# Optimization experiments

Measured on AMD Instinct MI355X. Metric: run time of the kernel, lower is better.

The kernel has to match this reference:

```python
import jax, jax.numpy as jnp
import numpy as np

B, S, DIM = 2, 1024, 1024
N_EXPERTS, K = 8, 2
VOCAB = 16384
HIDDEN = DIM * 8 // 3          # 2730
UP_OUT = HIDDEN * 2            # 5460 (swiglu doubling)


def setup_inputs() -> dict:
    key = jax.random.key(0)
    ks = jax.random.split(key, 5)
    x = jax.random.normal(ks[0], (B, S, DIM), dtype=jnp.float32)
    w_router = jax.random.normal(ks[1], (N_EXPERTS, DIM), dtype=jnp.float32) * 0.02
    w_up = jax.random.normal(ks[2], (N_EXPERTS, UP_OUT, DIM), dtype=jnp.float32) * 0.02
    w_down = jax.random.normal(ks[3], (N_EXPERTS, DIM, HIDDEN), dtype=jnp.float32) * 0.02
    w_proj = jax.random.normal(ks[4], (N_EXPERTS, VOCAB, DIM), dtype=jnp.float32) * 0.02
    return {"x": x, "w_router": w_router, "w_up": w_up, "w_down": w_down, "w_proj": w_proj}


def _grouped_linear(x_sorted, weight, group_sizes):
    # weight: [n_experts, out, in] (torch Linear layout) -> ragged_dot wants [g, in, out]
    return jax.lax.ragged_dot(x_sorted, jnp.swapaxes(weight, 1, 2), group_sizes)


def reference(x, w_router, w_up, w_down, w_proj):
    b, s, d = x.shape
    # Router (eval path): plain top-k of linear scores
    scores = jnp.einsum("bsd,nd->bsn", x, w_router)
    c, ids = jax.lax.top_k(scores, K)                   # [B,S,K]
    # Dispatch: replicate tokens k times, sort by expert id (stable, matching torch.sort)
    xe = jnp.broadcast_to(x[..., None, :], (b, s, K, d)).reshape(-1, d)   # [T, d]
    ids_flat = ids.reshape(-1)
    order = jnp.argsort(ids_flat)                        # stable sort indices
    x_sorted = xe[order]
    group_sizes = jnp.bincount(ids_flat, length=N_EXPERTS).astype(jnp.int32)
    # Expert swiglu MLP with residual (grouped GEMMs)
    skip = x_sorted
    h = _grouped_linear(x_sorted, w_up, group_sizes)     # [T, 2*HIDDEN]
    h_lin, h_gate = jnp.split(h, 2, axis=-1)
    h = h_lin * jax.nn.silu(h_gate)
    h = _grouped_linear(h, w_down, group_sizes) + skip   # [T, d]
    logits = _grouped_linear(h, w_proj, group_sizes)     # [T, VOCAB]
    # Postprocess: scatter back to original token order
    out = jnp.zeros_like(logits).at[order].set(logits)
    out = out.reshape(b, s, K, VOCAB)
    # Weighted top-k combine
    w = jax.nn.softmax(c, axis=-1)                       # [B,S,K]
    return jnp.sum(out * w[..., None], axis=-2)          # [B,S,VOCAB]
```

## Files before the change

### kernel.cpp

```cpp
#include <hip/hip_runtime.h>
#include <hip/hip_bf16.h>

typedef __bf16 bf16_t;
typedef __bf16 bf16x2 __attribute__((ext_vector_type(2)));
typedef __bf16 bf16x4 __attribute__((ext_vector_type(4)));
typedef __bf16 bf16x8 __attribute__((ext_vector_type(8)));
typedef float f32x4 __attribute__((ext_vector_type(4)));

#define DIM     1024
#define NEXP    8
#define VOCAB   16384
#define HIDDEN  2730
#define UPOUT   5460
#define NTOK    2048
#define NSLOT   4096
#define HRAW_LD 5472
#define H1_LD   2752
#define BM      256
#define MAXTILES 24

#define WS_COUNTS      0
#define WS_NTILES      64
#define WS_TILE_E      128
#define WS_TILE_M0     256
#define WS_TILE_MEND   384
#define WS_SLOT_IDS    1024
#define WS_SLOT_W      20480
#define WS_SLOT_OF_POS 40960
#define WS_POS_OF_SLOT 61440
#define WS_XSORTED     131072
#define WS_H2          8519680
#define WS_H1          16908288
#define WS_HRAW        39452672
#define WS_LOGITS      16908288ull
#define WS_NEED_BIG    (WS_LOGITS + (size_t)NSLOT * VOCAB * 2)

__device__ __forceinline__ void gload_lds16(const void* g, void* l) {
    __builtin_amdgcn_global_load_lds((const __attribute__((address_space(1))) void*)g,
                                     (__attribute__((address_space(3))) void*)l, 16, 0, 0);
}
__device__ __forceinline__ int swzm(int r) { return (r ^ (r >> 2)) & 3; }

__global__ __launch_bounds__(256) void router_kernel(const float* __restrict__ x,
        const float* __restrict__ wr, int* __restrict__ slot_ids,
        float* __restrict__ slot_w, int* __restrict__ counts) {
    const int lane = threadIdx.x & 63;
    const int wave = threadIdx.x >> 6;
    const int token = blockIdx.x * 4 + wave;
    const float* xrow = x + (size_t)token * DIM;
    float acc[NEXP];
#pragma unroll
    for (int e = 0; e < NEXP; ++e) acc[e] = 0.f;
#pragma unroll
    for (int i = 0; i < DIM / 64; ++i) {
        const int k = i * 64 + lane;
        const float xv = xrow[k];
#pragma unroll
        for (int e = 0; e < NEXP; ++e) acc[e] += xv * wr[e * DIM + k];
    }
#pragma unroll
    for (int off = 32; off > 0; off >>= 1) {
#pragma unroll
        for (int e = 0; e < NEXP; ++e) acc[e] += __shfl_xor(acc[e], off);
    }
    if (lane == 0) {
        float c0 = -1e30f; int b0 = 0;
#pragma unroll
        for (int e = 0; e < NEXP; ++e) if (acc[e] > c0) { c0 = acc[e]; b0 = e; }
        float c1 = -1e30f; int b1 = 0;
#pragma unroll
        for (int e = 0; e < NEXP; ++e) if (e != b0 && acc[e] > c1) { c1 = acc[e]; b1 = e; }
        slot_ids[token * 2 + 0] = b0;
        slot_ids[token * 2 + 1] = b1;
        const float w0 = 1.f / (1.f + expf(c1 - c0));
        slot_w[token * 2 + 0] = w0;
        slot_w[token * 2 + 1] = 1.f - w0;
        atomicAdd(&counts[b0], 1);
        atomicAdd(&counts[b1], 1);
    }
}

__global__ __launch_bounds__(512) void sched_kernel(const int* __restrict__ counts,
        int* __restrict__ ntiles, int* __restrict__ tile_e, int* __restrict__ tile_m0,
        int* __restrict__ tile_mend, const int* __restrict__ slot_ids,
        int* __restrict__ slot_of_pos, int* __restrict__ pos_of_slot) {
    __shared__ int offs[NEXP];
    if (threadIdx.x == 0) {
        int o = 0, nt = 0;
        for (int e = 0; e < NEXP; ++e) {
            offs[e] = o;
            const int c = counts[e];
            for (int m = 0; m < c; m += BM) {
                tile_e[nt] = e; tile_m0[nt] = o + m; tile_mend[nt] = o + c; ++nt;
            }
            o += c;
        }
        *ntiles = nt;
    }
    __syncthreads();
    const int e = threadIdx.x >> 6;
    const int lane = threadIdx.x & 63;
    int base = offs[e];
    for (int ch = 0; ch < NSLOT / 64; ++ch) {
        const int i = ch * 64 + lane;
        const int id = slot_ids[i];
        const unsigned long long m = __ballot(id == e);
        if (id == e) {
            const int rank = __popcll(m & ((1ull << lane) - 1ull));
            slot_of_pos[base + rank] = i;
            pos_of_slot[i] = base + rank;
        }
        base += __popcll(m);
    }
}

__global__ __launch_bounds__(256) void gather_kernel(const float* __restrict__ x,
        const int* __restrict__ slot_of_pos, bf16_t* __restrict__ xs) {
    const int row = blockIdx.x;
    const int t = threadIdx.x;
    const int tok = slot_of_pos[row] >> 1;
    const float4 v = *(const float4*)(x + (size_t)tok * DIM + t * 4);
    bf16x4 o;
    o.x = (bf16_t)v.x; o.y = (bf16_t)v.y; o.z = (bf16_t)v.z; o.w = (bf16_t)v.w;
    *(bf16x4*)(xs + (size_t)row * DIM + t * 4) = o;
}

__global__ __launch_bounds__(256) void swiglu_kernel(const bf16_t* __restrict__ hraw,
        bf16_t* __restrict__ h1) {
    const int row = blockIdx.x;
    const int col = blockIdx.y * 256 + threadIdx.x;
    if (col >= H1_LD) return;
    float o = 0.f;
    if (col < HIDDEN) {
        const float a = (float)hraw[(size_t)row * HRAW_LD + col];
        const float g = (float)hraw[(size_t)row * HRAW_LD + col + HIDDEN];
        o = a * (g / (1.f + expf(-g)));
    }
    h1[(size_t)row * H1_LD + col] = (bf16_t)o;
}

__global__ __launch_bounds__(256) void combine_kernel(const bf16_t* __restrict__ logits,
        const int* __restrict__ pos_of_slot, const float* __restrict__ slot_w,
        float* __restrict__ out) {
    const int t = blockIdx.x;
    const int v0 = (blockIdx.y * 256 + threadIdx.x) * 8;
    const int p0 = pos_of_slot[2 * t], p1 = pos_of_slot[2 * t + 1];
    const float w0 = slot_w[2 * t], w1 = slot_w[2 * t + 1];
    const bf16x8 a = *(const bf16x8*)(logits + (size_t)p0 * VOCAB + v0);
    const bf16x8 b = *(const bf16x8*)(logits + (size_t)p1 * VOCAB + v0);
    float o[8];
#pragma unroll
    for (int i = 0; i < 8; ++i) o[i] = w0 * (float)a[i] + w1 * (float)b[i];
    *(float4*)(out + (size_t)t * VOCAB + v0)     = make_float4(o[0], o[1], o[2], o[3]);
    *(float4*)(out + (size_t)t * VOCAB + v0 + 4) = make_float4(o[4], o[5], o[6], o[7]);
}

template <int EPI, bool BW16, int BN, bool SWZ>
__global__ __launch_bounds__(1024, 4) void gemm_kernel(
        const bf16_t* __restrict__ A, int lda,
        const float* __restrict__ B, int N, int K, int KT, long bLast,
        bf16_t* __restrict__ C, int ldc,
        const bf16_t* __restrict__ skip,
        const int* __restrict__ slot_of_pos,
        const float* __restrict__ slot_w,
        float* __restrict__ outp,
        const int* __restrict__ tile_e,
        const int* __restrict__ tile_m0,
        const int* __restrict__ tile_mend,
        const int* __restrict__ ntiles) {
    if (blockIdx.y >= (unsigned)*ntiles) return;
    int bx = blockIdx.x;
    if constexpr (SWZ) bx = (bx & 7) * (gridDim.x >> 3) + (bx >> 3);
    const int e = tile_e[blockIdx.y];
    const int m0 = tile_m0[blockIdx.y];
    const int mend = tile_mend[blockIdx.y];
    const int n0 = bx * BN;

    constexpr int NI = BN / 64;
    constexpr int NB = BW16 ? BN / 128 : 1;
    constexpr int VM = NB + 1;

    __shared__ bf16_t sA[2][BM][32];
    __shared__ bf16_t sB[2][BN][32];

    const int tid = threadIdx.x;
    const int lane = tid & 63;
    const int wave = tid >> 6;
    const int wr = wave >> 2;
    const int wc = wave & 3;
    const int fr = lane & 15;
    const int fq = lane >> 4;

    f32x4 acc[4][NI] = {};

    auto stageA = [&](int buf, int kt) {
        const int k0 = min(kt, KT - 1) * 32;
        const int rb = wave * 16;
        const int r = rb + (lane >> 2);
        const int gr = min(m0 + r, NSLOT - 1);
        const int c16 = (lane & 3) ^ swzm(r);
        gload_lds16(A + (size_t)gr * lda + k0 + c16 * 8, &sA[buf][rb][0]);
    };
    auto loadB = [&](int kt, f32x4* va, float2& vc) {
        const int k0 = min(kt, KT - 1) * 32;
        if constexpr (BW16) {
#pragma unroll
            for (int nb = 0; nb < NB; ++nb) {
                const int gr = min(n0 + nb * 128 + wave * 8 + (lane >> 3), N - 1);
                va[nb] = *(const f32x4*)(B + (size_t)e * N * K + (size_t)gr * K
                                         + k0 + (lane & 7) * 4);
            }
        } else {
            long fl = (long)e * N * K + (long)(n0 + wave * 4 + (lane >> 4)) * K
                      + k0 + (lane & 15) * 2;
            if (fl > bLast) fl = bLast;
            vc = *(const float2*)(B + fl);
        }
    };
    auto writeB = [&](int buf, const f32x4* va, const float2& vc) {
        if constexpr (BW16) {
#pragma unroll
            for (int nb = 0; nb < NB; ++nb) {
                const int r = nb * 128 + wave * 8 + (lane >> 3);
                bf16x4 t;
                t.x = (bf16_t)va[nb].x; t.y = (bf16_t)va[nb].y;
                t.z = (bf16_t)va[nb].z; t.w = (bf16_t)va[nb].w;
                char* p = (char*)&sB[buf][r][0]
                        + ((((lane & 7) >> 1) ^ swzm(r)) * 16) + (lane & 1) * 8;
                *(bf16x4*)p = t;
            }
        } else {
            const int r = wave * 4 + (lane >> 4);
            bf16x2 t; t.x = (bf16_t)vc.x; t.y = (bf16_t)vc.y;
            const int q = lane & 15;
            char* p = (char*)&sB[buf][r][0] + (((q >> 2) ^ swzm(r)) * 16) + (q & 3) * 4;
            *(bf16x2*)p = t;
        }
    };
    auto compute = [&](int buf) {
        bf16x8 bb[NI];
#pragma unroll
        for (int ni = 0; ni < NI; ++ni) {
            const int r = wc * (BN / 4) + ni * 16 + fr;
            bb[ni] = *(const bf16x8*)&sB[buf][r][(fq ^ swzm(r)) * 8];
        }
        __builtin_amdgcn_s_setprio(1);
#pragma unroll
        for (int mi = 0; mi < 4; ++mi) {
            const int r = wr * 64 + mi * 16 + fr;
            const bf16x8 af = *(const bf16x8*)&sA[buf][r][(fq ^ swzm(r)) * 8];
#pragma unroll
            for (int ni = 0; ni < NI; ++ni)
                acc[mi][ni] = __builtin_amdgcn_mfma_f32_16x16x32_bf16(
                        af, bb[ni], acc[mi][ni], 0, 0, 0);
        }
        __builtin_amdgcn_s_setprio(0);
    };

    f32x4 Pa[NB], Qa[NB]; float2 Pc, Qc;
    loadB(0, Pa, Pc);
    stageA(0, 0);
    loadB(1, Qa, Qc);
    asm volatile("s_waitcnt vmcnt(%0)" :: "n"(VM) : "memory");
    writeB(0, Pa, Pc);
    asm volatile("s_waitcnt lgkmcnt(0)" ::: "memory");
    stageA(1, 1);

    for (int kt = 0; kt < KT; kt += 2) {
        loadB(kt + 2, Pa, Pc);
        asm volatile("s_waitcnt vmcnt(%0)" :: "n"(VM) : "memory");
        __builtin_amdgcn_s_barrier();
        asm volatile("" ::: "memory");
        writeB(1, Qa, Qc);
        compute(0);
        asm volatile("s_waitcnt lgkmcnt(0)" ::: "memory");
        __builtin_amdgcn_s_barrier();
        asm volatile("" ::: "memory");
        stageA(0, kt + 2);
        loadB(kt + 3, Qa, Qc);
        asm volatile("s_waitcnt vmcnt(%0)" :: "n"(VM) : "memory");
        __builtin_amdgcn_s_barrier();
        asm volatile("" ::: "memory");
        writeB(0, Pa, Pc);
        compute(1);
        asm volatile("s_waitcnt lgkmcnt(0)" ::: "memory");
        __builtin_amdgcn_s_barrier();
        asm volatile("" ::: "memory");
        stageA(1, kt + 3);
    }

#pragma unroll
    for (int mi = 0; mi < 4; ++mi) {
#pragma unroll
        for (int reg = 0; reg < 4; ++reg) {
            const int r = m0 + wr * 64 + mi * 16 + fq * 4 + reg;
            if (r >= mend) continue;
            int tok = 0; float wgt = 0.f;
            if constexpr (EPI == 2) {
                const int slot = slot_of_pos[r];
                tok = slot >> 1;
                wgt = slot_w[slot];
            }
#pragma unroll
            for (int ni = 0; ni < NI; ++ni) {
                const int c = n0 + wc * (BN / 4) + ni * 16 + fr;
                if (c >= N) continue;
                float v = acc[mi][ni][reg];
                if constexpr (EPI == 0) {
                    C[(size_t)r * ldc + c] = (bf16_t)v;
                } else if constexpr (EPI == 1) {
                    v += (float)skip[(size_t)r * DIM + c];
                    C[(size_t)r * ldc + c] = (bf16_t)v;
                } else {
                    unsafeAtomicAdd(&outp[(size_t)tok * VOCAB + c], v * wgt);
                }
            }
        }
    }
}

extern "C" void kernel_launch(void* const* d_in, const int* in_sizes, int n_in,
                              void* d_out, int out_size, void* d_ws, size_t ws_size,
                              hipStream_t stream) {
    const float* x        = (const float*)d_in[0];
    const float* w_router = (const float*)d_in[1];
    const float* w_up     = (const float*)d_in[2];
    const float* w_down   = (const float*)d_in[3];
    const float* w_proj   = (const float*)d_in[4];
    float* out = (float*)d_out;
    char* ws = (char*)d_ws;

    int*    counts      = (int*)(ws + WS_COUNTS);
    int*    ntiles      = (int*)(ws + WS_NTILES);
    int*    tile_e      = (int*)(ws + WS_TILE_E);
    int*    tile_m0     = (int*)(ws + WS_TILE_M0);
    int*    tile_mend   = (int*)(ws + WS_TILE_MEND);
    int*    slot_ids    = (int*)(ws + WS_SLOT_IDS);
    float*  slot_w      = (float*)(ws + WS_SLOT_W);
    int*    slot_of_pos = (int*)(ws + WS_SLOT_OF_POS);
    int*    pos_of_slot = (int*)(ws + WS_POS_OF_SLOT);
    bf16_t* x_sorted    = (bf16_t*)(ws + WS_XSORTED);
    bf16_t* h2          = (bf16_t*)(ws + WS_H2);
    bf16_t* h1          = (bf16_t*)(ws + WS_H1);
    bf16_t* h_raw       = (bf16_t*)(ws + WS_HRAW);
    bf16_t* logits      = (bf16_t*)(ws + WS_LOGITS);

    const bool bigws = ws_size >= WS_NEED_BIG;

    hipMemsetAsync(d_ws, 0, 1024, stream);

    router_kernel<<<NTOK / 4, 256, 0, stream>>>(x, w_router, slot_ids, slot_w, counts);
    sched_kernel<<<1, 512, 0, stream>>>(counts, ntiles, tile_e, tile_m0, tile_mend,
                                        slot_ids, slot_of_pos, pos_of_slot);
    gather_kernel<<<NSLOT, 256, 0, stream>>>(x, slot_of_pos, x_sorted);

    gemm_kernel<0, true, 256, false><<<dim3((UPOUT + 255) / 256, MAXTILES), 1024, 0, stream>>>(
        x_sorted, DIM, w_up, UPOUT, DIM, 32, 0,
        h_raw, HRAW_LD,
        nullptr, nullptr, nullptr, nullptr, tile_e, tile_m0, tile_mend, ntiles);

    swiglu_kernel<<<dim3(NSLOT, (H1_LD + 255) / 256), 256, 0, stream>>>(h_raw, h1);

    gemm_kernel<1, false, 64, true><<<dim3(DIM / 64, MAXTILES), 1024, 0, stream>>>(
        h1, H1_LD, w_down, DIM, HIDDEN, (HIDDEN + 31) / 32,
        (long)NEXP * DIM * HIDDEN - 2,
        h2, DIM,
        x_sorted, nullptr, nullptr, nullptr, tile_e, tile_m0, tile_mend, ntiles);

    if (bigws) {
        gemm_kernel<0, true, 256, true><<<dim3(VOCAB / 256, MAXTILES), 1024, 0, stream>>>(
            h2, DIM, w_proj, VOCAB, DIM, 32, 0,
            logits, VOCAB,
            nullptr, nullptr, nullptr, nullptr, tile_e, tile_m0, tile_mend, ntiles);
        combine_kernel<<<dim3(NTOK, VOCAB / (256 * 8)), 256, 0, stream>>>(
            logits, pos_of_slot, slot_w, out);
    } else {
        hipMemsetAsync(d_out, 0, (size_t)out_size * sizeof(float), stream);
        gemm_kernel<2, true, 256, true><<<dim3(VOCAB / 256, MAXTILES), 1024, 0, stream>>>(
            h2, DIM, w_proj, VOCAB, DIM, 32, 0,
            nullptr, 0,
            nullptr, slot_of_pos, slot_w, out, tile_e, tile_m0, tile_mend, ntiles);
    }
}
```

Baseline: 631.4 us.

## Split GEMM into 512-thread high-reuse kernel and specialized mid kernel

Adds a dedicated gemm_hi kernel for the up and vocab projections. It uses 512 threads per block, so each wave computes an 8x4 grid of MFMA tiles instead of 4x4, which raises register-level reuse of the A and B fragments. Its B loads are rewritten so each thread reads 16 contiguous floats and writes them as two 16-byte bf16x8 stores to LDS. The down projection moves to a trimmed gemm_mid kernel that preloads all A fragments before the MFMA loop. The cost is higher register pressure in gemm_hi (128 accumulator floats per thread), fewer waves resident per CU, and more LDS work per thread.

```diff
diff --git a/kernel.cpp b/kernel.cpp
--- a/kernel.cpp
+++ b/kernel.cpp
@@ -155,15 +155,158 @@
     *(float4*)(out + (size_t)t * VOCAB + v0 + 4) = make_float4(o[4], o[5], o[6], o[7]);
 }
 
-template <int EPI, bool BW16, int BN, bool SWZ>
-__global__ __launch_bounds__(1024, 4) void gemm_kernel(
+template <int EPI, bool SWZ>
+__global__ __launch_bounds__(512, 2) void gemm_hi(
+        const bf16_t* __restrict__ A,
+        const float* __restrict__ B, int N,
+        bf16_t* __restrict__ C, int ldc,
+        const int* __restrict__ slot_of_pos,
+        const float* __restrict__ slot_w,
+        float* __restrict__ outp,
+        const int* __restrict__ tile_e,
+        const int* __restrict__ tile_m0,
+        const int* __restrict__ tile_mend,
+        const int* __restrict__ ntiles) {
+    if (blockIdx.y >= (unsigned)*ntiles) return;
+    constexpr int K = 1024, KT = 32;
+    int bx = blockIdx.x;
+    if constexpr (SWZ) bx = (bx & 7) * (gridDim.x >> 3) + (bx >> 3);
+    const int e = tile_e[blockIdx.y];
+    const int m0 = tile_m0[blockIdx.y];
+    const int mend = tile_mend[blockIdx.y];
+    const int n0 = bx * 256;
+    const float* __restrict__ Bexp = B + (size_t)e * N * K;
+
+    __shared__ bf16_t sA[2][256][32];
+    __shared__ bf16_t sB[2][256][32];
+
+    const int tid = threadIdx.x;
+    const int lane = tid & 63;
+    const int wave = tid >> 6;
+    const int wr = wave >> 2;
+    const int wc = wave & 3;
+    const int fr = lane & 15;
+    const int fq = lane >> 4;
+
+    const int brow = tid >> 1;
+    const int bseg = tid & 1;
+    const float* bsrc = Bexp + (size_t)min(n0 + brow, N - 1) * K + bseg * 16;
+
+    f32x4 acc[8][4] = {};
+
+    auto stageA = [&](int buf, int kt) {
+        const int k0 = min(kt, KT - 1) * 32;
+#pragma unroll
+        for (int j = 0; j < 2; ++j) {
+            const int rb = wave * 32 + j * 16;
+            const int r = rb + (lane >> 2);
+            const int gr = min(m0 + r, NSLOT - 1);
+            const int c16 = (lane & 3) ^ swzm(r);
+            gload_lds16(A + (size_t)gr * K + k0 + c16 * 8, &sA[buf][rb][0]);
+        }
+    };
+    auto loadB = [&](int kt, f32x4* v) {
+        const int k0 = min(kt, KT - 1) * 32;
+#pragma unroll
+        for (int j = 0; j < 4; ++j) v[j] = *(const f32x4*)(bsrc + k0 + j * 4);
+    };
+    auto writeB = [&](int buf, const f32x4* v) {
+#pragma unroll
+        for (int u = 0; u < 2; ++u) {
+            bf16x8 t;
+            t[0] = (bf16_t)v[2*u][0]; t[1] = (bf16_t)v[2*u][1];
+            t[2] = (bf16_t)v[2*u][2]; t[3] = (bf16_t)v[2*u][3];
+            t[4] = (bf16_t)v[2*u+1][0]; t[5] = (bf16_t)v[2*u+1][1];
+            t[6] = (bf16_t)v[2*u+1][2]; t[7] = (bf16_t)v[2*u+1][3];
+            const int unit = (bseg * 2 + u) ^ swzm(brow);
+            *(bf16x8*)&sB[buf][brow][unit * 8] = t;
+        }
+    };
+    auto compute = [&](int buf) {
+        bf16x8 bb[4];
+#pragma unroll
+        for (int ni = 0; ni < 4; ++ni) {
+            const int r = wc * 64 + ni * 16 + fr;
+            bb[ni] = *(const bf16x8*)&sB[buf][r][(fq ^ swzm(r)) * 8];
+        }
+        __builtin_amdgcn_s_setprio(1);
+#pragma unroll
+        for (int mi = 0; mi < 8; ++mi) {
+            const int r = wr * 128 + mi * 16 + fr;
+            const bf16x8 af = *(const bf16x8*)&sA[buf][r][(fq ^ swzm(r)) * 8];
+#pragma unroll
+            for (int ni = 0; ni < 4; ++ni)
+                acc[mi][ni] = __builtin_amdgcn_mfma_f32_16x16x32_bf16(
+                        af, bb[ni], acc[mi][ni], 0, 0, 0);
+        }
+        __builtin_amdgcn_s_setprio(0);
+    };
+
+    f32x4 P[4], Q[4];
+    loadB(0, P);
+    stageA(0, 0);
+    loadB(1, Q);
+    asm volatile("s_waitcnt vmcnt(6)" ::: "memory");
+    writeB(0, P);
+    asm volatile("s_waitcnt lgkmcnt(0)" ::: "memory");
+    stageA(1, 1);
+
+    for (int kt = 0; kt < KT; kt += 2) {
+        loadB(kt + 2, P);
+        asm volatile("s_waitcnt vmcnt(6)" ::: "memory");
+        __builtin_amdgcn_s_barrier();
+        asm volatile("" ::: "memory");
+        writeB(1, Q);
+        compute(0);
+        asm volatile("s_waitcnt lgkmcnt(0)" ::: "memory");
+        __builtin_amdgcn_s_barrier();
+        asm volatile("" ::: "memory");
+        stageA(0, kt + 2);
+        loadB(kt + 3, Q);
+        asm volatile("s_waitcnt vmcnt(6)" ::: "memory");
+        __builtin_amdgcn_s_barrier();
+        asm volatile("" ::: "memory");
+        writeB(0, P);
+        compute(1);
+        asm volatile("s_waitcnt lgkmcnt(0)" ::: "memory");
+        __builtin_amdgcn_s_barrier();
+        asm volatile("" ::: "memory");
+        stageA(1, kt + 3);
+    }
+
+#pragma unroll
+    for (int mi = 0; mi < 8; ++mi) {
+#pragma unroll
+        for (int reg = 0; reg < 4; ++reg) {
+            const int r = m0 + wr * 128 + mi * 16 + fq * 4 + reg;
+            if (r >= mend) continue;
+            int tok = 0; float wgt = 0.f;
+            if constexpr (EPI == 2) {
+                const int slot = slot_of_pos[r];
+                tok = slot >> 1;
+                wgt = slot_w[slot];
+            }
+#pragma unroll
+            for (int ni = 0; ni < 4; ++ni) {
+                const int c = n0 + wc * 64 + ni * 16 + fr;
+                if (c >= N) continue;
+                float v = acc[mi][ni][reg];
+                if constexpr (EPI == 0) {
+                    C[(size_t)r * ldc + c] = (bf16_t)v;
+                } else {
+                    unsafeAtomicAdd(&outp[(size_t)tok * VOCAB + c], v * wgt);
+                }
+            }
+        }
+    }
+}
+
+template <int EPI, int BN, bool SWZ>
+__global__ __launch_bounds__(1024, 4) void gemm_mid(
         const bf16_t* __restrict__ A, int lda,
         const float* __restrict__ B, int N, int K, int KT, long bLast,
         bf16_t* __restrict__ C, int ldc,
         const bf16_t* __restrict__ skip,
-        const int* __restrict__ slot_of_pos,
-        const float* __restrict__ slot_w,
-        float* __restrict__ outp,
         const int* __restrict__ tile_e,
         const int* __restrict__ tile_m0,
         const int* __restrict__ tile_mend,
@@ -177,8 +320,6 @@
     const int n0 = bx * BN;
 
     constexpr int NI = BN / 64;
-    constexpr int NB = BW16 ? BN / 128 : 1;
-    constexpr int VM = NB + 1;
 
     __shared__ bf16_t sA[2][BM][32];
     __shared__ bf16_t sB[2][BN][32];
@@ -201,44 +342,27 @@
         const int c16 = (lane & 3) ^ swzm(r);
         gload_lds16(A + (size_t)gr * lda + k0 + c16 * 8, &sA[buf][rb][0]);
     };
-    auto loadB = [&](int kt, f32x4* va, float2& vc) {
+    auto loadB = [&](int kt, float2& vc) {
         const int k0 = min(kt, KT - 1) * 32;
-        if constexpr (BW16) {
-#pragma unroll
-            for (int nb = 0; nb < NB; ++nb) {
-                const int gr = min(n0 + nb * 128 + wave * 8 + (lane >> 3), N - 1);
-                va[nb] = *(const f32x4*)(B + (size_t)e * N * K + (size_t)gr * K
-                                         + k0 + (lane & 7) * 4);
-            }
-        } else {
-            long fl = (long)e * N * K + (long)(n0 + wave * 4 + (lane >> 4)) * K
-                      + k0 + (lane & 15) * 2;
-            if (fl > bLast) fl = bLast;
-            vc = *(const float2*)(B + fl);
-        }
-    };
-    auto writeB = [&](int buf, const f32x4* va, const float2& vc) {
-        if constexpr (BW16) {
-#pragma unroll
-            for (int nb = 0; nb < NB; ++nb) {
-                const int r = nb * 128 + wave * 8 + (lane >> 3);
-                bf16x4 t;
-                t.x = (bf16_t)va[nb].x; t.y = (bf16_t)va[nb].y;
-                t.z = (bf16_t)va[nb].z; t.w = (bf16_t)va[nb].w;
-                char* p = (char*)&sB[buf][r][0]
-                        + ((((lane & 7) >> 1) ^ swzm(r)) * 16) + (lane & 1) * 8;
-                *(bf16x4*)p = t;
-            }
-        } else {
-            const int r = wave * 4 + (lane >> 4);
-            bf16x2 t; t.x = (bf16_t)vc.x; t.y = (bf16_t)vc.y;
-            const int q = lane & 15;
-            char* p = (char*)&sB[buf][r][0] + (((q >> 2) ^ swzm(r)) * 16) + (q & 3) * 4;
-            *(bf16x2*)p = t;
-        }
+        long fl = (long)e * N * K + (long)(n0 + wave * 4 + (lane >> 4)) * K
+                  + k0 + (lane & 15) * 2;
+        if (fl > bLast) fl = bLast;
+        vc = *(const float2*)(B + fl);
+    };
+    auto writeB = [&](int buf, const float2& vc) {
+        const int r = wave * 4 + (lane >> 4);
+        bf16x2 t; t.x = (bf16_t)vc.x; t.y = (bf16_t)vc.y;
+        const int q = lane & 15;
+        char* p = (char*)&sB[buf][r][0] + (((q >> 2) ^ swzm(r)) * 16) + (q & 3) * 4;
+        *(bf16x2*)p = t;
     };
     auto compute = [&](int buf) {
-        bf16x8 bb[NI];
+        bf16x8 af[4], bb[NI];
+#pragma unroll
+        for (int mi = 0; mi < 4; ++mi) {
+            const int r = wr * 64 + mi * 16 + fr;
+            af[mi] = *(const bf16x8*)&sA[buf][r][(fq ^ swzm(r)) * 8];
+        }
 #pragma unroll
         for (int ni = 0; ni < NI; ++ni) {
             const int r = wc * (BN / 4) + ni * 16 + fr;
@@ -246,42 +370,39 @@
         }
         __builtin_amdgcn_s_setprio(1);
 #pragma unroll
-        for (int mi = 0; mi < 4; ++mi) {
-            const int r = wr * 64 + mi * 16 + fr;
-            const bf16x8 af = *(const bf16x8*)&sA[buf][r][(fq ^ swzm(r)) * 8];
-#pragma unroll
-            for (int ni = 0; ni < NI; ++ni)
+        for (int ni = 0; ni < NI; ++ni)
+#pragma unroll
+            for (int mi = 0; mi < 4; ++mi)
                 acc[mi][ni] = __builtin_amdgcn_mfma_f32_16x16x32_bf16(
-                        af, bb[ni], acc[mi][ni], 0, 0, 0);
-        }
+                        af[mi], bb[ni], acc[mi][ni], 0, 0, 0);
         __builtin_amdgcn_s_setprio(0);
     };
 
-    f32x4 Pa[NB], Qa[NB]; float2 Pc, Qc;
-    loadB(0, Pa, Pc);
+    float2 Pc, Qc;
+    loadB(0, Pc);
     stageA(0, 0);
-    loadB(1, Qa, Qc);
-    asm volatile("s_waitcnt vmcnt(%0)" :: "n"(VM) : "memory");
-    writeB(0, Pa, Pc);
+    loadB(1, Qc);
+    asm volatile("s_waitcnt vmcnt(2)" ::: "memory");
+    writeB(0, Pc);
     asm volatile("s_waitcnt lgkmcnt(0)" ::: "memory");
     stageA(1, 1);
 
     for (int kt = 0; kt < KT; kt += 2) {
-        loadB(kt + 2, Pa, Pc);
-        asm volatile("s_waitcnt vmcnt(%0)" :: "n"(VM) : "memory");
-        __builtin_amdgcn_s_barrier();
-        asm volatile("" ::: "memory");
-        writeB(1, Qa, Qc);
+        loadB(kt + 2, Pc);
+        asm volatile("s_waitcnt vmcnt(2)" ::: "memory");
+        __builtin_amdgcn_s_barrier();
+        asm volatile("" ::: "memory");
+        writeB(1, Qc);
         compute(0);
         asm volatile("s_waitcnt lgkmcnt(0)" ::: "memory");
         __builtin_amdgcn_s_barrier();
         asm volatile("" ::: "memory");
         stageA(0, kt + 2);
-        loadB(kt + 3, Qa, Qc);
-        asm volatile("s_waitcnt vmcnt(%0)" :: "n"(VM) : "memory");
-        __builtin_amdgcn_s_barrier();
-        asm volatile("" ::: "memory");
-        writeB(0, Pa, Pc);
+        loadB(kt + 3, Qc);
+        asm volatile("s_waitcnt vmcnt(2)" ::: "memory");
+        __builtin_amdgcn_s_barrier();
+        asm volatile("" ::: "memory");
+        writeB(0, Pc);
         compute(1);
         asm volatile("s_waitcnt lgkmcnt(0)" ::: "memory");
         __builtin_amdgcn_s_barrier();
@@ -295,25 +416,13 @@
         for (int reg = 0; reg < 4; ++reg) {
             const int r = m0 + wr * 64 + mi * 16 + fq * 4 + reg;
             if (r >= mend) continue;
-            int tok = 0; float wgt = 0.f;
-            if constexpr (EPI == 2) {
-                const int slot = slot_of_pos[r];
-                tok = slot >> 1;
-                wgt = slot_w[slot];
-            }
 #pragma unroll
             for (int ni = 0; ni < NI; ++ni) {
                 const int c = n0 + wc * (BN / 4) + ni * 16 + fr;
                 if (c >= N) continue;
                 float v = acc[mi][ni][reg];
-                if constexpr (EPI == 0) {
-                    C[(size_t)r * ldc + c] = (bf16_t)v;
-                } else if constexpr (EPI == 1) {
-                    v += (float)skip[(size_t)r * DIM + c];
-                    C[(size_t)r * ldc + c] = (bf16_t)v;
-                } else {
-                    unsafeAtomicAdd(&outp[(size_t)tok * VOCAB + c], v * wgt);
-                }
+                if constexpr (EPI == 1) v += (float)skip[(size_t)r * DIM + c];
+                C[(size_t)r * ldc + c] = (bf16_t)v;
             }
         }
     }
@@ -354,31 +463,27 @@
                                         slot_ids, slot_of_pos, pos_of_slot);
     gather_kernel<<<NSLOT, 256, 0, stream>>>(x, slot_of_pos, x_sorted);
 
-    gemm_kernel<0, true, 256, false><<<dim3((UPOUT + 255) / 256, MAXTILES), 1024, 0, stream>>>(
-        x_sorted, DIM, w_up, UPOUT, DIM, 32, 0,
-        h_raw, HRAW_LD,
-        nullptr, nullptr, nullptr, nullptr, tile_e, tile_m0, tile_mend, ntiles);
+    gemm_hi<0, false><<<dim3((UPOUT + 255) / 256, MAXTILES), 512, 0, stream>>>(
+        x_sorted, w_up, UPOUT, h_raw, HRAW_LD,
+        nullptr, nullptr, nullptr, tile_e, tile_m0, tile_mend, ntiles);
 
     swiglu_kernel<<<dim3(NSLOT, (H1_LD + 255) / 256), 256, 0, stream>>>(h_raw, h1);
 
-    gemm_kernel<1, false, 64, true><<<dim3(DIM / 64, MAXTILES), 1024, 0, stream>>>(
+    gemm_mid<1, 64, true><<<dim3(DIM / 64, MAXTILES), 1024, 0, stream>>>(
         h1, H1_LD, w_down, DIM, HIDDEN, (HIDDEN + 31) / 32,
         (long)NEXP * DIM * HIDDEN - 2,
-        h2, DIM,
-        x_sorted, nullptr, nullptr, nullptr, tile_e, tile_m0, tile_mend, ntiles);
+        h2, DIM, x_sorted, tile_e, tile_m0, tile_mend, ntiles);
 
     if (bigws) {
-        gemm_kernel<0, true, 256, true><<<dim3(VOCAB / 256, MAXTILES), 1024, 0, stream>>>(
-            h2, DIM, w_proj, VOCAB, DIM, 32, 0,
-            logits, VOCAB,
-            nullptr, nullptr, nullptr, nullptr, tile_e, tile_m0, tile_mend, ntiles);
+        gemm_hi<0, true><<<dim3(VOCAB / 256, MAXTILES), 512, 0, stream>>>(
+            h2, w_proj, VOCAB, logits, VOCAB,
+            nullptr, nullptr, nullptr, tile_e, tile_m0, tile_mend, ntiles);
         combine_kernel<<<dim3(NTOK, VOCAB / (256 * 8)), 256, 0, stream>>>(
             logits, pos_of_slot, slot_w, out);
     } else {
         hipMemsetAsync(d_out, 0, (size_t)out_size * sizeof(float), stream);
-        gemm_kernel<2, true, 256, true><<<dim3(VOCAB / 256, MAXTILES), 1024, 0, stream>>>(
-            h2, DIM, w_proj, VOCAB, DIM, 32, 0,
-            nullptr, 0,
-            nullptr, slot_of_pos, slot_w, out, tile_e, tile_m0, tile_mend, ntiles);
-    }
-}
+        gemm_hi<2, true><<<dim3(VOCAB / 256, MAXTILES), 512, 0, stream>>>(
+            h2, w_proj, VOCAB, nullptr, 0,
+            slot_of_pos, slot_w, out, tile_e, tile_m0, tile_mend, ntiles);
+    }
+}
```

Result: slower. 706.2 us (+11.8%).

## Pre-convert projection weights to bf16 overlapped with up GEMM, use bf16-B GEMM

Applied to the files above, without the earlier changes.

Adds extra grid rows to the up-projection GEMM launch that convert w_proj from fp32 to bf16 into workspace, overlapping the conversion with that GEMM. The vocab projection then uses a new GEMM kernel that loads bf16 B tiles directly into LDS via global_load_lds, avoiding fp32 weight reads and in-register conversion in the largest GEMM. The cost is extra memory traffic for the conversion each call and a large additional workspace requirement, with a fallback to the old paths when the workspace is too small.

```diff
diff --git a/kernel.cpp b/kernel.cpp
--- a/kernel.cpp
+++ b/kernel.cpp
@@ -18,6 +18,7 @@
 #define H1_LD   2752
 #define BM      256
 #define MAXTILES 24
+#define CVT_Y   8
 
 #define WS_COUNTS      0
 #define WS_NTILES      64
@@ -34,6 +35,8 @@
 #define WS_HRAW        39452672
 #define WS_LOGITS      16908288ull
 #define WS_NEED_BIG    (WS_LOGITS + (size_t)NSLOT * VOCAB * 2)
+#define WS_WPROJ16     167772160ull
+#define WS_NEED2       (WS_WPROJ16 + (size_t)NEXP * VOCAB * DIM * 2)
 
 __device__ __forceinline__ void gload_lds16(const void* g, void* l) {
     __builtin_amdgcn_global_load_lds((const __attribute__((address_space(1))) void*)g,
@@ -155,7 +158,7 @@
     *(float4*)(out + (size_t)t * VOCAB + v0 + 4) = make_float4(o[4], o[5], o[6], o[7]);
 }
 
-template <int EPI, bool BW16, int BN, bool SWZ>
+template <int EPI, bool BW16, int BN, bool SWZ, bool CVT>
 __global__ __launch_bounds__(1024, 4) void gemm_kernel(
         const bf16_t* __restrict__ A, int lda,
         const float* __restrict__ B, int N, int K, int KT, long bLast,
@@ -167,7 +170,25 @@
         const int* __restrict__ tile_e,
         const int* __restrict__ tile_m0,
         const int* __restrict__ tile_mend,
-        const int* __restrict__ ntiles) {
+        const int* __restrict__ ntiles,
+        const float* __restrict__ cvt_src,
+        bf16_t* __restrict__ cvt_dst,
+        long cvt_n) {
+    if constexpr (CVT) {
+        if (blockIdx.y >= MAXTILES) {
+            const long nthr = (long)gridDim.x * 1024 * (gridDim.y - MAXTILES);
+            long gid = ((long)(blockIdx.y - MAXTILES) * gridDim.x + blockIdx.x) * 1024
+                       + threadIdx.x;
+            for (long i = gid * 4; i < cvt_n; i += nthr * 4) {
+                const f32x4 v = *(const f32x4*)(cvt_src + i);
+                bf16x4 o;
+                o.x = (bf16_t)v.x; o.y = (bf16_t)v.y;
+                o.z = (bf16_t)v.z; o.w = (bf16_t)v.w;
+                *(bf16x4*)(cvt_dst + i) = o;
+            }
+            return;
+        }
+    }
     if (blockIdx.y >= (unsigned)*ntiles) return;
     int bx = blockIdx.x;
     if constexpr (SWZ) bx = (bx & 7) * (gridDim.x >> 3) + (bx >> 3);
@@ -319,6 +340,97 @@
     }
 }
 
+template <bool SWZ>
+__global__ __launch_bounds__(1024, 4) void gemm_bb(
+        const bf16_t* __restrict__ A,
+        const bf16_t* __restrict__ Bb, int N, int K, int KT,
+        bf16_t* __restrict__ C, int ldc,
+        const int* __restrict__ tile_e,
+        const int* __restrict__ tile_m0,
+        const int* __restrict__ tile_mend,
+        const int* __restrict__ ntiles) {
+    if (blockIdx.y >= (unsigned)*ntiles) return;
+    int bx = blockIdx.x;
+    if constexpr (SWZ) bx = (bx & 7) * (gridDim.x >> 3) + (bx >> 3);
+    const int e = tile_e[blockIdx.y];
+    const int m0 = tile_m0[blockIdx.y];
+    const int mend = tile_mend[blockIdx.y];
+    const int n0 = bx * 256;
+    const bf16_t* __restrict__ Bexp = Bb + (size_t)e * N * K;
+
+    __shared__ bf16_t sA[2][256][32];
+    __shared__ bf16_t sB[2][256][32];
+
+    const int tid = threadIdx.x;
+    const int lane = tid & 63;
+    const int wave = tid >> 6;
+    const int wr = wave >> 2;
+    const int wc = wave & 3;
+    const int fr = lane & 15;
+    const int fq = lane >> 4;
+
+    const int rb  = wave * 16;
+    const int rr  = rb + (lane >> 2);
+    const int c16 = (lane & 3) ^ swzm(rr);
+    const int grA = min(m0 + rr, NSLOT - 1);
+    const int grB = min(n0 + rr, N - 1);
+
+    f32x4 acc[4][4] = {};
+
+    auto stage = [&](int buf, int kt) {
+        const int k0 = min(kt, KT - 1) * 32;
+        gload_lds16(A + (size_t)grA * K + k0 + c16 * 8, &sA[buf][rb][0]);
+        gload_lds16(Bexp + (size_t)grB * K + k0 + c16 * 8, &sB[buf][rb][0]);
+    };
+    auto compute = [&](int buf) {
+        bf16x8 bb[4];
+#pragma unroll
+        for (int ni = 0; ni < 4; ++ni) {
+            const int r = wc * 64 + ni * 16 + fr;
+            bb[ni] = *(const bf16x8*)&sB[buf][r][(fq ^ swzm(r)) * 8];
+        }
+        __builtin_amdgcn_s_setprio(1);
+#pragma unroll
+        for (int mi = 0; mi < 4; ++mi) {
+            const int r = wr * 64 + mi * 16 + fr;
+            const bf16x8 af = *(const bf16x8*)&sA[buf][r][(fq ^ swzm(r)) * 8];
+#pragma unroll
+            for (int ni = 0; ni < 4; ++ni)
+                acc[mi][ni] = __builtin_amdgcn_mfma_f32_16x16x32_bf16(
+                        af, bb[ni], acc[mi][ni], 0, 0, 0);
+        }
+        __builtin_amdgcn_s_setprio(0);
+    };
+
+    stage(0, 0);
+    stage(1, 1);
+    for (int kt = 0; kt < KT; ++kt) {
+        asm volatile("s_waitcnt vmcnt(2)" ::: "memory");
+        __builtin_amdgcn_s_barrier();
+        asm volatile("" ::: "memory");
+        compute(kt & 1);
+        asm volatile("s_waitcnt lgkmcnt(0)" ::: "memory");
+        __builtin_amdgcn_s_barrier();
+        asm volatile("" ::: "memory");
+        stage(kt & 1, kt + 2);
+    }
+
+#pragma unroll
+    for (int mi = 0; mi < 4; ++mi) {
+#pragma unroll
+        for (int reg = 0; reg < 4; ++reg) {
+            const int r = m0 + wr * 64 + mi * 16 + fq * 4 + reg;
+            if (r >= mend) continue;
+#pragma unroll
+            for (int ni = 0; ni < 4; ++ni) {
+                const int c = n0 + wc * 64 + ni * 16 + fr;
+                if (c >= N) continue;
+                C[(size_t)r * ldc + c] = (bf16_t)acc[mi][ni][reg];
+            }
+        }
+    }
+}
+
 extern "C" void kernel_launch(void* const* d_in, const int* in_sizes, int n_in,
                               void* d_out, int out_size, void* d_ws, size_t ws_size,
                               hipStream_t stream) {
@@ -344,8 +456,10 @@
     bf16_t* h1          = (bf16_t*)(ws + WS_H1);
     bf16_t* h_raw       = (bf16_t*)(ws + WS_HRAW);
     bf16_t* logits      = (bf16_t*)(ws + WS_LOGITS);
-
-    const bool bigws = ws_size >= WS_NEED_BIG;
+    bf16_t* wproj16     = (bf16_t*)(ws + WS_WPROJ16);
+
+    const bool bigws  = ws_size >= WS_NEED_BIG;
+    const bool bigws2 = ws_size >= WS_NEED2;
 
     hipMemsetAsync(d_ws, 0, 1024, stream);
 
@@ -354,31 +468,51 @@
                                         slot_ids, slot_of_pos, pos_of_slot);
     gather_kernel<<<NSLOT, 256, 0, stream>>>(x, slot_of_pos, x_sorted);
 
-    gemm_kernel<0, true, 256, false><<<dim3((UPOUT + 255) / 256, MAXTILES), 1024, 0, stream>>>(
-        x_sorted, DIM, w_up, UPOUT, DIM, 32, 0,
-        h_raw, HRAW_LD,
-        nullptr, nullptr, nullptr, nullptr, tile_e, tile_m0, tile_mend, ntiles);
+    if (bigws2) {
+        gemm_kernel<0, true, 256, false, true>
+            <<<dim3((UPOUT + 255) / 256, MAXTILES + CVT_Y), 1024, 0, stream>>>(
+            x_sorted, DIM, w_up, UPOUT, DIM, 32, 0,
+            h_raw, HRAW_LD,
+            nullptr, nullptr, nullptr, nullptr, tile_e, tile_m0, tile_mend, ntiles,
+            w_proj, wproj16, (long)NEXP * VOCAB * DIM);
+    } else {
+        gemm_kernel<0, true, 256, false, false>
+            <<<dim3((UPOUT + 255) / 256, MAXTILES), 1024, 0, stream>>>(
+            x_sorted, DIM, w_up, UPOUT, DIM, 32, 0,
+            h_raw, HRAW_LD,
+            nullptr, nullptr, nullptr, nullptr, tile_e, tile_m0, tile_mend, ntiles,
+            nullptr, nullptr, 0);
+    }
 
     swiglu_kernel<<<dim3(NSLOT, (H1_LD + 255) / 256), 256, 0, stream>>>(h_raw, h1);
 
-    gemm_kernel<1, false, 64, true><<<dim3(DIM / 64, MAXTILES), 1024, 0, stream>>>(
+    gemm_kernel<1, false, 64, true, false><<<dim3(DIM / 64, MAXTILES), 1024, 0, stream>>>(
         h1, H1_LD, w_down, DIM, HIDDEN, (HIDDEN + 31) / 32,
         (long)NEXP * DIM * HIDDEN - 2,
         h2, DIM,
-        x_sorted, nullptr, nullptr, nullptr, tile_e, tile_m0, tile_mend, ntiles);
-
-    if (bigws) {
-        gemm_kernel<0, true, 256, true><<<dim3(VOCAB / 256, MAXTILES), 1024, 0, stream>>>(
+        x_sorted, nullptr, nullptr, nullptr, tile_e, tile_m0, tile_mend, ntiles,
+        nullptr, nullptr, 0);
+
+    if (bigws2) {
+        gemm_bb<true><<<dim3(VOCAB / 256, MAXTILES), 1024, 0, stream>>>(
+            h2, wproj16, VOCAB, DIM, 32,
+            logits, VOCAB, tile_e, tile_m0, tile_mend, ntiles);
+        combine_kernel<<<dim3(NTOK, VOCAB / (256 * 8)), 256, 0, stream>>>(
+            logits, pos_of_slot, slot_w, out);
+    } else if (bigws) {
+        gemm_kernel<0, true, 256, true, false><<<dim3(VOCAB / 256, MAXTILES), 1024, 0, stream>>>(
             h2, DIM, w_proj, VOCAB, DIM, 32, 0,
             logits, VOCAB,
-            nullptr, nullptr, nullptr, nullptr, tile_e, tile_m0, tile_mend, ntiles);
+            nullptr, nullptr, nullptr, nullptr, tile_e, tile_m0, tile_mend, ntiles,
+            nullptr, nullptr, 0);
         combine_kernel<<<dim3(NTOK, VOCAB / (256 * 8)), 256, 0, stream>>>(
             logits, pos_of_slot, slot_w, out);
     } else {
         hipMemsetAsync(d_out, 0, (size_t)out_size * sizeof(float), stream);
-        gemm_kernel<2, true, 256, true><<<dim3(VOCAB / 256, MAXTILES), 1024, 0, stream>>>(
+        gemm_kernel<2, true, 256, true, false><<<dim3(VOCAB / 256, MAXTILES), 1024, 0, stream>>>(
             h2, DIM, w_proj, VOCAB, DIM, 32, 0,
             nullptr, 0,
-            nullptr, slot_of_pos, slot_w, out, tile_e, tile_m0, tile_mend, ntiles);
-    }
-}
+            nullptr, slot_of_pos, slot_w, out, tile_e, tile_m0, tile_mend, ntiles,
+            nullptr, nullptr, 0);
+    }
+}
```

After: 764.0 us. +21.0%, slower.
